# Kernel optimization log

Measured on AMD Instinct MI355X. Metric: run time of the kernel, lower is better.

## Reference

```python
import jax, jax.numpy as jnp
import numpy as np

NUM_HEADS = 16
HEAD_DIM = 128
EMBED = NUM_HEADS * HEAD_DIM  # 2048
BATCH, SEQ = 2, 2048


def setup_inputs() -> dict:
    key = jax.random.key(0)
    k1, k2 = jax.random.split(key)
    x = jax.random.normal(k1, (BATCH, SEQ, EMBED), dtype=jnp.float32)
    W = jax.random.normal(k2, (EMBED, 3 * EMBED), dtype=jnp.float32) * 0.02
    b = jnp.zeros((3 * EMBED,), dtype=jnp.float32)
    return {"x": x, "W": W, "b": b}


def _rotate_half(u):
    u1, u2 = jnp.split(u, 2, axis=-1)
    return jnp.concatenate([-u2, u1], axis=-1)


def reference(x, W, b):
    B, S, E = x.shape
    H, D = NUM_HEADS, HEAD_DIM
    # Fused QKV projection: [B,S,E] @ [E,3E] -> [B,S,3E]
    qkv = jnp.einsum('bse,ef->bsf', x, W) + b
    qkv = qkv.reshape(B, S, 3, H, D)
    q, k, v = qkv[:, :, 0], qkv[:, :, 1], qkv[:, :, 2]  # each [B,S,H,D]
    # Module's rotary embedding: sin/cos over arange(S*D), shared across heads
    t = jnp.arange(S * D, dtype=jnp.float32).reshape(1, S, 1, D)
    sin, cos = jnp.sin(t), jnp.cos(t)
    q = q * cos + _rotate_half(q) * sin
    k = k * cos + _rotate_half(k) * sin
    # Scaled dot-product attention over sequence, per head
    scale = 1.0 / jnp.sqrt(jnp.float32(D))
    attn = jnp.einsum('bqhd,bkhd->bhqk', q, k) * scale  # [B,H,S,S]
    w = jax.nn.softmax(attn, axis=-1)
    out = jnp.einsum('bhqk,bkhd->bqhd', w, v)  # [B,S,H,D]
    return out
```

## Files before the change

kernel.cpp:

```cpp
#include <hip/hip_runtime.h>
#include <stdint.h>

typedef unsigned short u16;
typedef __attribute__((ext_vector_type(8))) short bf16x8;
typedef __attribute__((ext_vector_type(4))) float f32x4;

#define NUM_B 2
#define SEQ   2048
#define SEQP  2080
#define NH    16
#define HD    128
#define EMB   2048
#define N3    6144
#define MM    4096
#define QT    64
#define WQ    32
#define KT    32
#define NTILE (SEQ / KT)

__device__ __forceinline__ u16 f2bf(float f) {
  union { float f; unsigned u; } c; c.f = f;
  return (u16)((c.u + 0x7FFFu + ((c.u >> 16) & 1u)) >> 16);
}
__device__ __forceinline__ void async16(const void* g, void* l) {
  __builtin_amdgcn_global_load_lds(
      (const __attribute__((address_space(1))) void*)g,
      (__attribute__((address_space(3))) void*)l, 16, 0, 0);
}


__global__ void k_cvt_bf16(const float* __restrict__ in, u16* __restrict__ out, int n4) {
  int i = blockIdx.x * blockDim.x + threadIdx.x;
  if (i >= n4) return;
  const float4 v = ((const float4*)in)[i];
  ushort4 o;
  o.x = f2bf(v.x); o.y = f2bf(v.y); o.z = f2bf(v.z); o.w = f2bf(v.w);
  ((ushort4*)out)[i] = o;
}

__global__ void k_transpose_w(const float* __restrict__ W, u16* __restrict__ Wt) {
  __shared__ float t[32][33];
  int n0 = blockIdx.x * 32, k0 = blockIdx.y * 32;
  int tx = threadIdx.x, ty = threadIdx.y;
  #pragma unroll
  for (int i = ty; i < 32; i += 8)
    t[i][tx] = W[(size_t)(k0 + i) * N3 + n0 + tx];
  __syncthreads();
  #pragma unroll
  for (int i = ty; i < 32; i += 8)
    Wt[(size_t)(n0 + i) * EMB + k0 + tx] = f2bf(t[tx][i]);
}

__global__ void k_sincos(float2* __restrict__ tab) {
  int i = blockIdx.x * blockDim.x + threadIdx.x;
  double t = (double)i;
  tab[i] = make_float2((float)cos(t), (float)sin(t));
}

__global__ __launch_bounds__(256, 2) void k_gemm_qkv(
    const u16* __restrict__ xb, const u16* __restrict__ wt,
    const float* __restrict__ bias, const float2* __restrict__ tab,
    u16* __restrict__ qb, u16* __restrict__ kb, u16* __restrict__ vbt)
{
  __shared__ __align__(16) u16 lsA[128 * 32];
  __shared__ __align__(16) u16 lsB[128 * 32];
  const int tid = threadIdx.x;
  const int wave = tid >> 6, lane = tid & 63;
  const int lq = lane & 15, lr = lane >> 4;
  const int m0 = blockIdx.y * 128, n0 = blockIdx.x * 128;

  f32x4 acc[2][8];
  #pragma unroll
  for (int i = 0; i < 2; ++i)
    #pragma unroll
    for (int j = 0; j < 8; ++j)
      acc[i][j] = f32x4{0.f, 0.f, 0.f, 0.f};

  for (int kt = 0; kt < EMB; kt += 32) {
    __syncthreads();
    #pragma unroll
    for (int i = 0; i < 2; ++i) {
      int c = tid + i * 256;
      async16(xb + (size_t)(m0 + (c >> 2)) * EMB + kt + (c & 3) * 8, lsA + c * 8);
      async16(wt + (size_t)(n0 + (c >> 2)) * EMB + kt + (c & 3) * 8, lsB + c * 8);
    }
    __syncthreads();
    bf16x8 af[2], bfr[8];
    #pragma unroll
    for (int i = 0; i < 2; ++i)
      af[i] = *(const bf16x8*)(lsA + (wave * 32 + i * 16 + lq) * 32 + lr * 8);
    #pragma unroll
    for (int j = 0; j < 8; ++j)
      bfr[j] = *(const bf16x8*)(lsB + (j * 16 + lq) * 32 + lr * 8);
    #pragma unroll
    for (int i = 0; i < 2; ++i)
      #pragma unroll
      for (int j = 0; j < 8; ++j)
        acc[i][j] = __builtin_amdgcn_mfma_f32_16x16x32_bf16(af[i], bfr[j], acc[i][j], 0, 0, 0);
  }

  const int w = n0 >> 11;
  const int h = (n0 & 2047) >> 7;
  float bb[8];
  #pragma unroll
  for (int j = 0; j < 8; ++j) bb[j] = bias[n0 + j * 16 + lq];

  if (w == 2) {
    #pragma unroll
    for (int i = 0; i < 2; ++i)
      #pragma unroll
      for (int j = 0; j < 8; ++j) {
        int d = j * 16 + lq;
        int mg0 = m0 + wave * 32 + i * 16 + lr * 4;
        int b = mg0 >> 11, s0 = mg0 & 2047;
        ushort4 pk;
        pk.x = f2bf(acc[i][j][0] + bb[j]);
        pk.y = f2bf(acc[i][j][1] + bb[j]);
        pk.z = f2bf(acc[i][j][2] + bb[j]);
        pk.w = f2bf(acc[i][j][3] + bb[j]);
        *(ushort4*)(vbt + ((size_t)(b * NH + h) * HD + d) * SEQP + s0) = pk;
      }
  } else {
    u16* basep = (w == 0) ? qb : kb;
    const float qs = (w == 0) ? 0.12751569843736827f : 1.0f;
    #pragma unroll
    for (int i = 0; i < 2; ++i)
      #pragma unroll
      for (int jp = 0; jp < 4; ++jp)
        #pragma unroll
        for (int r = 0; r < 4; ++r) {
          int row = wave * 32 + i * 16 + lr * 4 + r;
          int mg = m0 + row;
          int b = mg >> 11, s = mg & 2047;
          int d1 = jp * 16 + lq;
          float c1 = acc[i][jp][r]     + bb[jp];
          float c2 = acc[i][jp + 4][r] + bb[jp + 4];
          float2 s1 = tab[s * HD + d1];
          float2 s2 = tab[s * HD + d1 + 64];
          u16* dst = basep + ((size_t)(b * NH + h) * SEQ + s) * HD;
          dst[d1]      = f2bf((c1 * s1.x - c2 * s1.y) * qs);
          dst[d1 + 64] = f2bf((c2 * s2.x + c1 * s2.y) * qs);
        }
  }
}

__global__ __launch_bounds__(128, 2) void k_flash(
    const u16* __restrict__ qb, const u16* __restrict__ kb,
    const u16* __restrict__ vbt, float* __restrict__ out)
{
  __shared__ __align__(16) u16 lsK[2][KT * HD];
  __shared__ __align__(16) u16 lsV[2][HD * KT];
  __shared__ __align__(16) u16 lsP[2][WQ * KT];

  const int tid = threadIdx.x;
  const int wave = tid >> 6, lane = tid & 63;
  const int lq = lane & 15, lr = lane >> 4;
  const int i = blockIdx.x;
  const int xcd = i & 7, j = i >> 3;
  const int bh = xcd * 4 + (j >> 5);
  const int q0 = (j & 31) * QT;
  const u16* Qg = qb + ((size_t)bh * SEQ + q0 + wave * WQ) * HD;
  const u16* Kg = kb + (size_t)bh * SEQ * HD;
  const u16* Vg = vbt + (size_t)bh * HD * SEQP;

  auto stage = [&](int tile, int buf) {
    const int k0 = tile * KT;
    #pragma unroll
    for (int ii = 0; ii < 4; ++ii) {
      int c = tid + ii * 128;
      int key = c >> 4, grp = c & 15;
      async16(Kg + (size_t)(k0 + key) * HD + ((grp ^ (key & 7)) * 8), lsK[buf] + c * 8);
    }
    #pragma unroll
    for (int ii = 0; ii < 4; ++ii) {
      int c = tid + ii * 128;
      int d = c >> 2, g2 = c & 3;
      async16(Vg + (size_t)d * SEQP + k0 + ((g2 ^ ((d >> 1) & 3)) * 8), lsV[buf] + c * 8);
    }
  };

  stage(0, 0);

  bf16x8 qf[2][4];
  #pragma unroll
  for (int qq = 0; qq < 2; ++qq)
    #pragma unroll
    for (int ks = 0; ks < 4; ++ks)
      qf[qq][ks] = *(const bf16x8*)(Qg + (size_t)(qq * 16 + lq) * HD + ks * 32 + lr * 8);

  f32x4 acc_o[2][8];
  float lsum[2] = {0.f, 0.f};
  #pragma unroll
  for (int mb = 0; mb < 2; ++mb)
    #pragma unroll
    for (int nb = 0; nb < 8; ++nb) acc_o[mb][nb] = f32x4{0.f, 0.f, 0.f, 0.f};

  for (int t = 0; t < NTILE; ++t) {
    const int p = t & 1;
    __syncthreads();
    if (t + 1 < NTILE) stage(t + 1, 1 - p);

    f32x4 sacc[2][2];
    #pragma unroll
    for (int kbi = 0; kbi < 2; ++kbi)
      #pragma unroll
      for (int qq = 0; qq < 2; ++qq) sacc[kbi][qq] = f32x4{0.f, 0.f, 0.f, 0.f};
    #pragma unroll
    for (int ks = 0; ks < 4; ++ks) {
      bf16x8 kf[2];
      #pragma unroll
      for (int kbi = 0; kbi < 2; ++kbi) {
        int key = kbi * 16 + lq;
        int g = (ks * 4 + lr) ^ (key & 7);
        kf[kbi] = *(const bf16x8*)(lsK[p] + key * HD + g * 8);
      }
      #pragma unroll
      for (int kbi = 0; kbi < 2; ++kbi)
        #pragma unroll
        for (int qq = 0; qq < 2; ++qq)
          sacc[kbi][qq] = __builtin_amdgcn_mfma_f32_16x16x32_bf16(kf[kbi], qf[qq][ks], sacc[kbi][qq], 0, 0, 0);
    }

    #pragma unroll
    for (int kbi = 0; kbi < 2; ++kbi)
      #pragma unroll
      for (int qq = 0; qq < 2; ++qq) {
        float p0 = __builtin_amdgcn_exp2f(sacc[kbi][qq][0]);
        float p1 = __builtin_amdgcn_exp2f(sacc[kbi][qq][1]);
        float p2 = __builtin_amdgcn_exp2f(sacc[kbi][qq][2]);
        float p3 = __builtin_amdgcn_exp2f(sacc[kbi][qq][3]);
        lsum[qq] += (p0 + p1) + (p2 + p3);
        int row = qq * 16 + lq;
        int g = kbi * 4 + lr;
        int gp = g ^ (row & 6);
        uint2 pk;
        pk.x = (uint32_t)f2bf(p0) | ((uint32_t)f2bf(p1) << 16);
        pk.y = (uint32_t)f2bf(p2) | ((uint32_t)f2bf(p3) << 16);
        *(uint2*)(lsP[wave] + row * KT + gp * 4) = pk;
      }

    bf16x8 ap[2];
    #pragma unroll
    for (int mb = 0; mb < 2; ++mb) {
      int row = mb * 16 + lq;
      int gp = (2 * lr) ^ (row & 6);
      ap[mb] = *(const bf16x8*)(lsP[wave] + row * KT + gp * 4);
    }
    #pragma unroll
    for (int nb = 0; nb < 8; ++nb) {
      int d = nb * 16 + lq;
      int g2 = lr ^ ((d >> 1) & 3);
      bf16x8 bv = *(const bf16x8*)(lsV[p] + d * KT + g2 * 8);
      #pragma unroll
      for (int mb = 0; mb < 2; ++mb)
        acc_o[mb][nb] = __builtin_amdgcn_mfma_f32_16x16x32_bf16(ap[mb], bv[0] == bv[0] ? bv : bv, acc_o[mb][nb], 0, 0, 0);
    }
  }

  float inv[2];
  #pragma unroll
  for (int qq = 0; qq < 2; ++qq) {
    float s = lsum[qq];
    s += __shfl_xor(s, 16);
    s += __shfl_xor(s, 32);
    inv[qq] = 1.0f / s;
  }
  const int b = bh >> 4, h = bh & 15;
  #pragma unroll
  for (int mb = 0; mb < 2; ++mb)
    #pragma unroll
    for (int r = 0; r < 4; ++r) {
      float iv = __shfl(inv[mb], lr * 4 + r);
      int row = wave * WQ + mb * 16 + lr * 4 + r;
      int sq = q0 + row;
      float* op = out + (((size_t)b * SEQ + sq) * NH + h) * HD;
      #pragma unroll
      for (int nb = 0; nb < 8; ++nb)
        op[nb * 16 + lq] = acc_o[mb][nb][r] * iv;
    }
}


extern "C" void kernel_launch(void* const* d_in, const int* in_sizes, int n_in,
                              void* d_out, int out_size, void* d_ws, size_t ws_size,
                              hipStream_t stream) {
  (void)in_sizes; (void)n_in; (void)out_size; (void)ws_size;
  const float* x    = (const float*)d_in[0];
  const float* W    = (const float*)d_in[1];
  const float* bias = (const float*)d_in[2];
  float* out = (float*)d_out;

  char* p = (char*)d_ws;
  u16* xb  = (u16*)p;  p += (size_t)MM * EMB * 2;
  u16* wt  = (u16*)p;  p += (size_t)N3 * EMB * 2;
  u16* qb  = (u16*)p;  p += (size_t)NUM_B * NH * SEQ * HD * 2;
  u16* kb  = (u16*)p;  p += (size_t)NUM_B * NH * SEQ * HD * 2;
  u16* vbt = (u16*)p;  p += (size_t)NUM_B * NH * HD * SEQP * 2;
  float2* tab = (float2*)p;

  k_cvt_bf16<<<(MM * EMB / 4 + 255) / 256, 256, 0, stream>>>(x, xb, MM * EMB / 4);
  k_transpose_w<<<dim3(N3 / 32, EMB / 32), dim3(32, 8), 0, stream>>>(W, wt);
  k_sincos<<<(SEQ * HD) / 256, 256, 0, stream>>>(tab);
  k_gemm_qkv<<<dim3(N3 / 128, MM / 128), 256, 0, stream>>>(xb, wt, bias, tab, qb, kb, vbt);
  k_flash<<<SEQ / QT * NUM_B * NH, 128, 0, stream>>>(qb, kb, vbt, out);
}
```

Measured before the change: 252.2 us.

## Rewrite QKV GEMM with larger tiles, double-buffered async LDS loads and swizzle

The QKV projection GEMM moves from a 128x128x32 single-buffered tile with 256 threads to a 128x256x64 tile with 512 threads. LDS is double-buffered, with global-to-LDS prefetch of the next A and B tiles issued during compute. An XOR swizzle is applied to the LDS layout to avoid bank conflicts, and MFMA sections run under raised wave priority. The epilogue is remapped to the new wave layout. This aims to hide global load latency and raise MFMA utilisation, at the cost of more LDS (96KB) and manual waitcnt/barrier sequencing that must be correct.

```diff
diff --git a/kernel.cpp b/kernel.cpp
--- a/kernel.cpp
+++ b/kernel.cpp
@@ -18,6 +18,11 @@
 #define KT    32
 #define NTILE (SEQ / KT)
 
+#define BM 128
+#define BN 256
+#define BK 64
+#define NT_K (EMB / BK)
+
 __device__ __forceinline__ u16 f2bf(float f) {
   union { float f; unsigned u; } c; c.f = f;
   return (u16)((c.u + 0x7FFFu + ((c.u >> 16) & 1u)) >> 16);
@@ -27,6 +32,9 @@
       (const __attribute__((address_space(1))) void*)g,
       (__attribute__((address_space(3))) void*)l, 16, 0, 0);
 }
+
+#define GBAR()   asm volatile("s_barrier" ::: "memory")
+#define WLGKM0() asm volatile("s_waitcnt lgkmcnt(0)" ::: "memory")
 
 
 __global__ void k_cvt_bf16(const float* __restrict__ in, u16* __restrict__ out, int n4) {
@@ -57,90 +65,156 @@
   tab[i] = make_float2((float)cos(t), (float)sin(t));
 }
 
-__global__ __launch_bounds__(256, 2) void k_gemm_qkv(
+__global__ __launch_bounds__(512, 2) void k_gemm_qkv(
     const u16* __restrict__ xb, const u16* __restrict__ wt,
     const float* __restrict__ bias, const float2* __restrict__ tab,
     u16* __restrict__ qb, u16* __restrict__ kb, u16* __restrict__ vbt)
 {
-  __shared__ __align__(16) u16 lsA[128 * 32];
-  __shared__ __align__(16) u16 lsB[128 * 32];
+  __shared__ __align__(16) u16 lsA[2][BM * BK];
+  __shared__ __align__(16) u16 lsB[2][BN * BK];
   const int tid = threadIdx.x;
   const int wave = tid >> 6, lane = tid & 63;
   const int lq = lane & 15, lr = lane >> 4;
-  const int m0 = blockIdx.y * 128, n0 = blockIdx.x * 128;
-
-  f32x4 acc[2][8];
-  #pragma unroll
-  for (int i = 0; i < 2; ++i)
-    #pragma unroll
-    for (int j = 0; j < 8; ++j)
+  const int wr = wave >> 2, wc = wave & 3;
+  const int m0 = blockIdx.y * BM, n0 = blockIdx.x * BN;
+
+  auto stageA = [&](int t, int buf) {
+    const int kt = t * BK;
+    #pragma unroll
+    for (int ii = 0; ii < 2; ++ii) {
+      int s = ii * 512 + tid;
+      int row = s >> 3, gq = (s & 7) ^ (row & 7);
+      async16(xb + (size_t)(m0 + row) * EMB + kt + gq * 8, &lsA[buf][s * 8]);
+    }
+  };
+  auto stageB = [&](int t, int buf, int half) {
+    const int kt = t * BK;
+    #pragma unroll
+    for (int ii = 0; ii < 2; ++ii) {
+      int s = ii * 512 + tid;
+      int row = s >> 3, gq = (s & 7) ^ (row & 7);
+      async16(wt + (size_t)(n0 + half * 128 + row) * EMB + kt + gq * 8,
+              &lsB[buf][half * 8192 + s * 8]);
+    }
+  };
+
+  f32x4 acc[4][4];
+  #pragma unroll
+  for (int i = 0; i < 4; ++i)
+    #pragma unroll
+    for (int j = 0; j < 4; ++j)
       acc[i][j] = f32x4{0.f, 0.f, 0.f, 0.f};
 
-  for (int kt = 0; kt < EMB; kt += 32) {
-    __syncthreads();
-    #pragma unroll
-    for (int i = 0; i < 2; ++i) {
-      int c = tid + i * 256;
-      async16(xb + (size_t)(m0 + (c >> 2)) * EMB + kt + (c & 3) * 8, lsA + c * 8);
-      async16(wt + (size_t)(n0 + (c >> 2)) * EMB + kt + (c & 3) * 8, lsB + c * 8);
-    }
-    __syncthreads();
-    bf16x8 af[2], bfr[8];
-    #pragma unroll
-    for (int i = 0; i < 2; ++i)
-      af[i] = *(const bf16x8*)(lsA + (wave * 32 + i * 16 + lq) * 32 + lr * 8);
-    #pragma unroll
-    for (int j = 0; j < 8; ++j)
-      bfr[j] = *(const bf16x8*)(lsB + (j * 16 + lq) * 32 + lr * 8);
-    #pragma unroll
-    for (int i = 0; i < 2; ++i)
-      #pragma unroll
-      for (int j = 0; j < 8; ++j)
-        acc[i][j] = __builtin_amdgcn_mfma_f32_16x16x32_bf16(af[i], bfr[j], acc[i][j], 0, 0, 0);
+  int rbase[4];
+  #pragma unroll
+  for (int nf = 0; nf < 4; ++nf)
+    rbase[nf] = ((wc >> 1) * 128 + (nf >> 1) * 64 + (wc & 1) * 32 + (nf & 1) * 16 + lq) * BK;
+  const int aRow0 = (wr * 64 + lq) * BK;
+  int qsw[2];
+  qsw[0] = ((0 + lr) ^ (lq & 7)) * 8;
+  qsw[1] = ((4 + lr) ^ (lq & 7)) * 8;
+
+  stageA(0, 0); stageB(0, 0, 0); stageB(0, 0, 1);
+  stageB(1, 1, 0); stageB(1, 1, 1);
+  asm volatile("s_waitcnt vmcnt(4)" ::: "memory");
+  GBAR();
+
+  for (int t = 0; t < NT_K; ++t) {
+    const int p = t & 1;
+    const u16* Ap = lsA[p];
+    const u16* Bp = lsB[p];
+    bf16x8 bfr[4][2];
+
+    #pragma unroll
+    for (int q = 0; q < 2; ++q) {
+      bf16x8 afr[2][2];
+      if (q == 0) {
+        #pragma unroll
+        for (int nf = 0; nf < 4; ++nf)
+          #pragma unroll
+          for (int kk = 0; kk < 2; ++kk)
+            bfr[nf][kk] = *(const bf16x8*)(Bp + rbase[nf] + qsw[kk]);
+      }
+      #pragma unroll
+      for (int mfl = 0; mfl < 2; ++mfl)
+        #pragma unroll
+        for (int kk = 0; kk < 2; ++kk)
+          afr[mfl][kk] = *(const bf16x8*)(Ap + aRow0 + (q * 32 + mfl * 16) * BK + qsw[kk]);
+
+      if (q == 0) {
+        if (t + 1 < NT_K) stageA(t + 1, 1 - p);
+      } else {
+        if (t + 2 < NT_K) {
+          stageB(t + 2, p, 0);
+          stageB(t + 2, p, 1);
+          asm volatile("s_waitcnt vmcnt(4)" ::: "memory");
+        } else if (t + 1 < NT_K) {
+          asm volatile("s_waitcnt vmcnt(0)" ::: "memory");
+        }
+      }
+      GBAR();
+      WLGKM0();
+      __builtin_amdgcn_s_setprio(1);
+      #pragma unroll
+      for (int kk = 0; kk < 2; ++kk)
+        #pragma unroll
+        for (int mfl = 0; mfl < 2; ++mfl)
+          #pragma unroll
+          for (int nf = 0; nf < 4; ++nf)
+            acc[q * 2 + mfl][nf] = __builtin_amdgcn_mfma_f32_16x16x32_bf16(
+                afr[mfl][kk], bfr[nf][kk], acc[q * 2 + mfl][nf], 0, 0, 0);
+      __builtin_amdgcn_s_setprio(0);
+      GBAR();
+    }
   }
 
   const int w = n0 >> 11;
-  const int h = (n0 & 2047) >> 7;
-  float bb[8];
-  #pragma unroll
-  for (int j = 0; j < 8; ++j) bb[j] = bias[n0 + j * 16 + lq];
+  const int h = ((n0 & 2047) >> 7) + (wc >> 1);
+  float bb[4];
+  int dloc[4];
+  #pragma unroll
+  for (int nf = 0; nf < 4; ++nf) {
+    dloc[nf] = (nf >> 1) * 64 + (wc & 1) * 32 + (nf & 1) * 16 + lq;
+    bb[nf] = bias[n0 + (wc >> 1) * 128 + dloc[nf]];
+  }
 
   if (w == 2) {
     #pragma unroll
-    for (int i = 0; i < 2; ++i)
-      #pragma unroll
-      for (int j = 0; j < 8; ++j) {
-        int d = j * 16 + lq;
-        int mg0 = m0 + wave * 32 + i * 16 + lr * 4;
-        int b = mg0 >> 11, s0 = mg0 & 2047;
+    for (int mfg = 0; mfg < 4; ++mfg) {
+      int mg0 = m0 + wr * 64 + mfg * 16 + lr * 4;
+      int b = mg0 >> 11, s0 = mg0 & 2047;
+      #pragma unroll
+      for (int nf = 0; nf < 4; ++nf) {
+        int d = dloc[nf];
         ushort4 pk;
-        pk.x = f2bf(acc[i][j][0] + bb[j]);
-        pk.y = f2bf(acc[i][j][1] + bb[j]);
-        pk.z = f2bf(acc[i][j][2] + bb[j]);
-        pk.w = f2bf(acc[i][j][3] + bb[j]);
+        pk.x = f2bf(acc[mfg][nf][0] + bb[nf]);
+        pk.y = f2bf(acc[mfg][nf][1] + bb[nf]);
+        pk.z = f2bf(acc[mfg][nf][2] + bb[nf]);
+        pk.w = f2bf(acc[mfg][nf][3] + bb[nf]);
         *(ushort4*)(vbt + ((size_t)(b * NH + h) * HD + d) * SEQP + s0) = pk;
       }
+    }
   } else {
     u16* basep = (w == 0) ? qb : kb;
     const float qs = (w == 0) ? 0.12751569843736827f : 1.0f;
     #pragma unroll
-    for (int i = 0; i < 2; ++i)
-      #pragma unroll
-      for (int jp = 0; jp < 4; ++jp)
-        #pragma unroll
-        for (int r = 0; r < 4; ++r) {
-          int row = wave * 32 + i * 16 + lr * 4 + r;
-          int mg = m0 + row;
-          int b = mg >> 11, s = mg & 2047;
-          int d1 = jp * 16 + lq;
-          float c1 = acc[i][jp][r]     + bb[jp];
-          float c2 = acc[i][jp + 4][r] + bb[jp + 4];
+    for (int mfg = 0; mfg < 4; ++mfg)
+      #pragma unroll
+      for (int r = 0; r < 4; ++r) {
+        int mg = m0 + wr * 64 + mfg * 16 + lr * 4 + r;
+        int b = mg >> 11, s = mg & 2047;
+        u16* dst = basep + ((size_t)(b * NH + h) * SEQ + s) * HD;
+        #pragma unroll
+        for (int nf = 0; nf < 2; ++nf) {
+          int d1 = dloc[nf];
+          float c1 = acc[mfg][nf][r]     + bb[nf];
+          float c2 = acc[mfg][nf + 2][r] + bb[nf + 2];
           float2 s1 = tab[s * HD + d1];
           float2 s2 = tab[s * HD + d1 + 64];
-          u16* dst = basep + ((size_t)(b * NH + h) * SEQ + s) * HD;
           dst[d1]      = f2bf((c1 * s1.x - c2 * s1.y) * qs);
           dst[d1 + 64] = f2bf((c2 * s2.x + c1 * s2.y) * qs);
         }
+      }
   }
 }
 
@@ -301,6 +375,6 @@
   k_cvt_bf16<<<(MM * EMB / 4 + 255) / 256, 256, 0, stream>>>(x, xb, MM * EMB / 4);
   k_transpose_w<<<dim3(N3 / 32, EMB / 32), dim3(32, 8), 0, stream>>>(W, wt);
   k_sincos<<<(SEQ * HD) / 256, 256, 0, stream>>>(tab);
-  k_gemm_qkv<<<dim3(N3 / 128, MM / 128), 256, 0, stream>>>(xb, wt, bias, tab, qb, kb, vbt);
+  k_gemm_qkv<<<dim3(N3 / BN, MM / BM), 512, 0, stream>>>(xb, wt, bias, tab, qb, kb, vbt);
   k_flash<<<SEQ / QT * NUM_B * NH, 128, 0, stream>>>(qb, kb, vbt, out);
 }
```

Result: slower. 260.2 us (+3.2%).

## Enlarge QKV GEMM tiles to 256x384 with double-buffered swizzled LDS

Applied to the files above, without the earlier changes.

Rewrites the QKV projection GEMM to use 256x384x64 block tiles, with each wave computing a 128x192 sub-tile. LDS is double-buffered so the next K tile's async global-to-LDS loads overlap the current tile's MFMAs, and an XOR swizzle on 16-byte chunks is meant to avoid LDS bank conflicts. The goal is more data reuse per byte loaded and fewer barriers per FLOP. In exchange it needs a very large accumulator register set (96 f32x4), runs at occupancy 1, and launches only 16x16=256 blocks, which may underfill the GPU.

```diff
diff --git a/kernel.cpp b/kernel.cpp
--- a/kernel.cpp
+++ b/kernel.cpp
@@ -18,6 +18,11 @@
 #define KT    32
 #define NTILE (SEQ / KT)
 
+#define BM 256
+#define BN 384
+#define BK 64
+#define NT_K (EMB / BK)
+
 __device__ __forceinline__ u16 f2bf(float f) {
   union { float f; unsigned u; } c; c.f = f;
   return (u16)((c.u + 0x7FFFu + ((c.u >> 16) & 1u)) >> 16);
@@ -27,6 +32,9 @@
       (const __attribute__((address_space(1))) void*)g,
       (__attribute__((address_space(3))) void*)l, 16, 0, 0);
 }
+
+#define GBAR()  asm volatile("s_barrier" ::: "memory")
+#define WVM0()  asm volatile("s_waitcnt vmcnt(0)" ::: "memory")
 
 
 __global__ void k_cvt_bf16(const float* __restrict__ in, u16* __restrict__ out, int n4) {
@@ -57,90 +65,141 @@
   tab[i] = make_float2((float)cos(t), (float)sin(t));
 }
 
-__global__ __launch_bounds__(256, 2) void k_gemm_qkv(
+__global__ __launch_bounds__(256, 1) void k_gemm_qkv(
     const u16* __restrict__ xb, const u16* __restrict__ wt,
     const float* __restrict__ bias, const float2* __restrict__ tab,
     u16* __restrict__ qb, u16* __restrict__ kb, u16* __restrict__ vbt)
 {
-  __shared__ __align__(16) u16 lsA[128 * 32];
-  __shared__ __align__(16) u16 lsB[128 * 32];
+  __shared__ __align__(16) u16 lsA[2][BM * BK];
+  __shared__ __align__(16) u16 lsB[2][BN * BK];
   const int tid = threadIdx.x;
   const int wave = tid >> 6, lane = tid & 63;
   const int lq = lane & 15, lr = lane >> 4;
-  const int m0 = blockIdx.y * 128, n0 = blockIdx.x * 128;
-
-  f32x4 acc[2][8];
-  #pragma unroll
-  for (int i = 0; i < 2; ++i)
-    #pragma unroll
-    for (int j = 0; j < 8; ++j)
+  const int wr = wave >> 1, wc = wave & 1;
+  const int m0 = blockIdx.y * BM, n0 = blockIdx.x * BN;
+
+  auto stA = [&](int t) {
+    const int kt = t * BK;
+    u16* dst = lsA[t & 1];
+    #pragma unroll
+    for (int ii = 0; ii < 8; ++ii) {
+      int s = ii * 256 + tid;
+      int row = s >> 3, gq = (s & 7) ^ (row & 7);
+      async16(xb + (size_t)(m0 + row) * EMB + kt + gq * 8, dst + s * 8);
+    }
+  };
+  auto stB = [&](int t) {
+    const int kt = t * BK;
+    u16* dst = lsB[t & 1];
+    #pragma unroll
+    for (int ii = 0; ii < 12; ++ii) {
+      int s = ii * 256 + tid;
+      int row = s >> 3, gq = (s & 7) ^ (row & 7);
+      async16(wt + (size_t)(n0 + row) * EMB + kt + gq * 8, dst + s * 8);
+    }
+  };
+
+  f32x4 acc[8][12];
+  #pragma unroll
+  for (int i = 0; i < 8; ++i)
+    #pragma unroll
+    for (int j = 0; j < 12; ++j)
       acc[i][j] = f32x4{0.f, 0.f, 0.f, 0.f};
 
-  for (int kt = 0; kt < EMB; kt += 32) {
-    __syncthreads();
-    #pragma unroll
-    for (int i = 0; i < 2; ++i) {
-      int c = tid + i * 256;
-      async16(xb + (size_t)(m0 + (c >> 2)) * EMB + kt + (c & 3) * 8, lsA + c * 8);
-      async16(wt + (size_t)(n0 + (c >> 2)) * EMB + kt + (c & 3) * 8, lsB + c * 8);
-    }
-    __syncthreads();
-    bf16x8 af[2], bfr[8];
-    #pragma unroll
-    for (int i = 0; i < 2; ++i)
-      af[i] = *(const bf16x8*)(lsA + (wave * 32 + i * 16 + lq) * 32 + lr * 8);
-    #pragma unroll
-    for (int j = 0; j < 8; ++j)
-      bfr[j] = *(const bf16x8*)(lsB + (j * 16 + lq) * 32 + lr * 8);
-    #pragma unroll
-    for (int i = 0; i < 2; ++i)
-      #pragma unroll
-      for (int j = 0; j < 8; ++j)
-        acc[i][j] = __builtin_amdgcn_mfma_f32_16x16x32_bf16(af[i], bfr[j], acc[i][j], 0, 0, 0);
-  }
-
-  const int w = n0 >> 11;
-  const int h = (n0 & 2047) >> 7;
-  float bb[8];
-  #pragma unroll
-  for (int j = 0; j < 8; ++j) bb[j] = bias[n0 + j * 16 + lq];
-
-  if (w == 2) {
-    #pragma unroll
-    for (int i = 0; i < 2; ++i)
-      #pragma unroll
-      for (int j = 0; j < 8; ++j) {
-        int d = j * 16 + lq;
-        int mg0 = m0 + wave * 32 + i * 16 + lr * 4;
+  int rbase[12];
+  #pragma unroll
+  for (int nf = 0; nf < 12; ++nf) {
+    int g = nf >> 1, half = nf & 1;
+    int pg = 6 * wc + g;
+    int col = (pg >> 2) * 128 + (pg & 3) * 16 + half * 64 + lq;
+    rbase[nf] = col * BK;
+  }
+  const int aRow0 = (wr * 128 + lq) * BK;
+  int qsw[2];
+  qsw[0] = ((0 + lr) ^ (lq & 7)) * 8;
+  qsw[1] = ((4 + lr) ^ (lq & 7)) * 8;
+
+  stA(0); stB(0);
+
+  for (int t = 0; t < NT_K; ++t) {
+    WVM0();
+    GBAR();
+    if (t + 1 < NT_K) { stA(t + 1); stB(t + 1); }
+
+    const u16* Ap = lsA[t & 1];
+    const u16* Bp = lsB[t & 1];
+
+    #pragma unroll
+    for (int kk = 0; kk < 2; ++kk) {
+      bf16x8 af[8];
+      #pragma unroll
+      for (int mf = 0; mf < 8; ++mf)
+        af[mf] = *(const bf16x8*)(Ap + aRow0 + (mf * 16) * BK + qsw[kk]);
+      #pragma unroll
+      for (int tt = 0; tt < 2; ++tt) {
+        bf16x8 bfr[6];
+        #pragma unroll
+        for (int z = 0; z < 6; ++z)
+          bfr[z] = *(const bf16x8*)(Bp + rbase[tt * 6 + z] + qsw[kk]);
+        #pragma unroll
+        for (int mf = 0; mf < 8; ++mf)
+          #pragma unroll
+          for (int z = 0; z < 6; ++z)
+            acc[mf][tt * 6 + z] = __builtin_amdgcn_mfma_f32_16x16x32_bf16(
+                af[mf], bfr[z], acc[mf][tt * 6 + z], 0, 0, 0);
+      }
+    }
+  }
+
+  const int m0w = m0 + wr * 128;
+  const int bxH = n0 >> 7;
+  #pragma unroll
+  for (int g = 0; g < 6; ++g) {
+    const int pg = 6 * wc + g;
+    const int j = pg >> 2;
+    const int s4 = pg & 3;
+    const int H = bxH + j;
+    const int w = H >> 4;
+    const int h = H & 15;
+    const int d1 = s4 * 16 + lq;
+    const float b1 = bias[n0 + j * 128 + d1];
+    const float b2 = bias[n0 + j * 128 + d1 + 64];
+
+    if (w == 2) {
+      #pragma unroll
+      for (int mf = 0; mf < 8; ++mf) {
+        int mg0 = m0w + mf * 16 + lr * 4;
         int b = mg0 >> 11, s0 = mg0 & 2047;
         ushort4 pk;
-        pk.x = f2bf(acc[i][j][0] + bb[j]);
-        pk.y = f2bf(acc[i][j][1] + bb[j]);
-        pk.z = f2bf(acc[i][j][2] + bb[j]);
-        pk.w = f2bf(acc[i][j][3] + bb[j]);
-        *(ushort4*)(vbt + ((size_t)(b * NH + h) * HD + d) * SEQP + s0) = pk;
+        pk.x = f2bf(acc[mf][2 * g][0] + b1);
+        pk.y = f2bf(acc[mf][2 * g][1] + b1);
+        pk.z = f2bf(acc[mf][2 * g][2] + b1);
+        pk.w = f2bf(acc[mf][2 * g][3] + b1);
+        *(ushort4*)(vbt + ((size_t)(b * NH + h) * HD + d1) * SEQP + s0) = pk;
+        pk.x = f2bf(acc[mf][2 * g + 1][0] + b2);
+        pk.y = f2bf(acc[mf][2 * g + 1][1] + b2);
+        pk.z = f2bf(acc[mf][2 * g + 1][2] + b2);
+        pk.w = f2bf(acc[mf][2 * g + 1][3] + b2);
+        *(ushort4*)(vbt + ((size_t)(b * NH + h) * HD + d1 + 64) * SEQP + s0) = pk;
       }
-  } else {
-    u16* basep = (w == 0) ? qb : kb;
-    const float qs = (w == 0) ? 0.12751569843736827f : 1.0f;
-    #pragma unroll
-    for (int i = 0; i < 2; ++i)
-      #pragma unroll
-      for (int jp = 0; jp < 4; ++jp)
+    } else {
+      u16* basep = (w == 0) ? qb : kb;
+      const float qs = (w == 0) ? 0.12751569843736827f : 1.0f;
+      #pragma unroll
+      for (int mf = 0; mf < 8; ++mf)
         #pragma unroll
         for (int r = 0; r < 4; ++r) {
-          int row = wave * 32 + i * 16 + lr * 4 + r;
-          int mg = m0 + row;
+          int mg = m0w + mf * 16 + lr * 4 + r;
           int b = mg >> 11, s = mg & 2047;
-          int d1 = jp * 16 + lq;
-          float c1 = acc[i][jp][r]     + bb[jp];
-          float c2 = acc[i][jp + 4][r] + bb[jp + 4];
+          u16* dst = basep + ((size_t)(b * NH + h) * SEQ + s) * HD;
+          float c1 = acc[mf][2 * g][r]     + b1;
+          float c2 = acc[mf][2 * g + 1][r] + b2;
           float2 s1 = tab[s * HD + d1];
           float2 s2 = tab[s * HD + d1 + 64];
-          u16* dst = basep + ((size_t)(b * NH + h) * SEQ + s) * HD;
           dst[d1]      = f2bf((c1 * s1.x - c2 * s1.y) * qs);
           dst[d1 + 64] = f2bf((c2 * s2.x + c1 * s2.y) * qs);
         }
+    }
   }
 }
 
@@ -301,6 +360,6 @@
   k_cvt_bf16<<<(MM * EMB / 4 + 255) / 256, 256, 0, stream>>>(x, xb, MM * EMB / 4);
   k_transpose_w<<<dim3(N3 / 32, EMB / 32), dim3(32, 8), 0, stream>>>(W, wt);
   k_sincos<<<(SEQ * HD) / 256, 256, 0, stream>>>(tab);
-  k_gemm_qkv<<<dim3(N3 / 128, MM / 128), 256, 0, stream>>>(xb, wt, bias, tab, qb, kb, vbt);
+  k_gemm_qkv<<<dim3(N3 / BN, MM / BM), 256, 0, stream>>>(xb, wt, bias, tab, qb, kb, vbt);
   k_flash<<<SEQ / QT * NUM_B * NH, 128, 0, stream>>>(qb, kb, vbt, out);
 }
```

Result: slower. 809.1 us (+220.8%).
